# Kernel optimization log

Hardware: AMD Instinct MI355X
Metric: run time of the kernel (lower is better)

Reference implementation:

```python
import jax, jax.numpy as jnp
import numpy as np

B, D, H, L, T = 4096, 1024, 2048, 256, 8
STD = 0.02


def setup_inputs() -> dict:
    key = jax.random.key(0)
    ks = jax.random.split(key, 24)
    n = lambda k, shp: (jax.random.normal(k, shp, dtype=jnp.float32) * STD)
    inp = {
        "x": jax.random.uniform(ks[0], (B, D), dtype=jnp.float32),
        "task": jax.random.randint(ks[1], (B,), 0, T),
        "eps": jax.random.normal(ks[2], (B, L), dtype=jnp.float32),
        # per-task encoder stacks: in->H->H->H->2L
        "enc_W1": n(ks[3], (T, D, H)), "enc_b1": jnp.zeros((T, H)),
        "enc_W2": n(ks[4], (T, H, H)), "enc_b2": jnp.zeros((T, H)),
        "enc_W3": n(ks[5], (T, H, H)), "enc_b3": jnp.zeros((T, H)),
        "enc_W4": n(ks[6], (T, H, 2 * L)), "enc_b4": jnp.zeros((T, 2 * L)),
        # shared decoder (BayesianLinear means): L->H->H
        "ds_W1": n(ks[7], (L, H)), "ds_b1": jnp.zeros((H,)),
        "ds_W2": n(ks[8], (H, H)), "ds_b2": jnp.zeros((H,)),
        # per-task decoder heads: H->H->D with Sigmoid
        "hd_W1": n(ks[9], (T, H, H)), "hd_b1": jnp.zeros((T, H)),
        "hd_W2": n(ks[10], (T, H, D)), "hd_b2": jnp.zeros((T, D)),
    }
    return inp


def reference(x, task, eps,
              enc_W1, enc_b1, enc_W2, enc_b2, enc_W3, enc_b3, enc_W4, enc_b4,
              ds_W1, ds_b1, ds_W2, ds_b2,
              hd_W1, hd_b1, hd_W2, hd_b2):
    ntasks = enc_W1.shape[0]
    onehot = jax.nn.one_hot(task, ntasks, dtype=x.dtype)  # [B, T], the task==idx mask

    # ---- encode: run every task's encoder on the full batch, mask-sum ----
    def enc_one(W1, b1, W2, b2, W3, b3, W4, b4):
        h = jax.nn.relu(x @ W1 + b1)
        h = jax.nn.relu(h @ W2 + b2)
        h = jax.nn.relu(h @ W3 + b3)
        return h @ W4 + b4  # [B, 2L]

    enc_all = jax.vmap(enc_one)(enc_W1, enc_b1, enc_W2, enc_b2,
                                enc_W3, enc_b3, enc_W4, enc_b4)  # [T, B, 2L]
    scat = jnp.einsum('tbd,bt->bd', enc_all, onehot)  # [B, 2L]
    latent = scat.shape[1] // 2
    mu, log_sigma = scat[:, :latent], scat[:, latent:]
    z = mu + jnp.exp(log_sigma) * eps  # reparameterization

    # ---- decode: shared trunk, then every head masked ----
    h = jax.nn.relu(z @ ds_W1 + ds_b1)
    h = jax.nn.relu(h @ ds_W2 + ds_b2)  # [B, H]

    def head_one(W1, b1, W2, b2):
        g = jax.nn.relu(h @ W1 + b1)
        return jax.nn.sigmoid(g @ W2 + b2)  # [B, D]

    heads_all = jax.vmap(head_one)(hd_W1, hd_b1, hd_W2, hd_b2)  # [T, B, D]
    return jnp.einsum('tbd,bt->bd', heads_all, onehot)  # [B, D]
```

## Files before the change

### kernel.cpp

```cpp
#include <hip/hip_runtime.h>
#include <hip/hip_bf16.h>

#define T_TASKS 8
#define B_ROWS 4096
#define PADROWS 4224
#define BM 128
#define BN 128
#define BK 32
#define MAXTILES 40

typedef __attribute__((ext_vector_type(4))) float f32x4;
typedef __attribute__((ext_vector_type(8))) short bf16x8;

#define GLOAD_LDS16(g, l) __builtin_amdgcn_global_load_lds( \
    (const __attribute__((address_space(1))) void*)(g), \
    (__attribute__((address_space(3))) void*)(l), 16, 0, 0)

struct TP { const float* src; unsigned short* dst; int K; int N; int ntiles; };

__device__ __forceinline__ unsigned short f32_to_bf16(float f) {
    union { float f; unsigned int u; } v; v.f = f;
    unsigned int r = v.u + 0x7FFF + ((v.u >> 16) & 1);
    return (unsigned short)(r >> 16);
}

__global__ void setup_kernel(const int* __restrict__ task, int* __restrict__ perm,
                             int* __restrict__ offs, int* __restrict__ table) {
    __shared__ int cnt[T_TASKS];
    __shared__ int cur[T_TASKS];
    int tid = threadIdx.x;
    if (tid < T_TASKS) cnt[tid] = 0;
    __syncthreads();
    for (int b = tid; b < B_ROWS; b += blockDim.x)
        atomicAdd(&cnt[task[b]], 1);
    __syncthreads();
    if (tid == 0) {
        int o = 0;
        for (int t = 0; t < T_TASKS; ++t) { offs[t] = o; cur[t] = o; o += cnt[t]; }
        offs[T_TASKS] = o;
        int s = 0;
        for (int t = 0; t < T_TASKS; ++t) {
            int nt = (cnt[t] + BM - 1) / BM;
            for (int j = 0; j < nt; ++j) table[s++] = (t << 16) | j;
        }
        for (; s < MAXTILES; ++s) table[s] = -1;
    }
    __syncthreads();
    for (int b = tid; b < B_ROWS; b += blockDim.x) {
        int t = task[b];
        int pos = atomicAdd(&cur[t], 1);
        perm[pos] = b;
    }
}

__global__ void permute_cast_kernel(const float* __restrict__ x, const int* __restrict__ perm,
                                    unsigned short* __restrict__ xp) {
    int rowp = blockIdx.x;
    int src = perm[rowp];
    const float4* xin = reinterpret_cast<const float4*>(x + (size_t)src * 1024);
    unsigned short* dst = xp + (size_t)rowp * 1024;
    int c4 = threadIdx.x;
    float4 v = xin[c4];
    ushort4 o;
    o.x = f32_to_bf16(v.x); o.y = f32_to_bf16(v.y);
    o.z = f32_to_bf16(v.z); o.w = f32_to_bf16(v.w);
    *reinterpret_cast<ushort4*>(dst + c4 * 4) = o;
}

__global__ void vae_kernel(const float* __restrict__ scat, const float* __restrict__ eps,
                           const int* __restrict__ perm, unsigned short* __restrict__ z) {
    int rowp = blockIdx.x;
    int c = threadIdx.x;
    int src = perm[rowp];
    float mu = scat[(size_t)rowp * 512 + c];
    float ls = scat[(size_t)rowp * 512 + 256 + c];
    float e  = eps[(size_t)src * 256 + c];
    z[(size_t)rowp * 256 + c] = f32_to_bf16(mu + __expf(ls) * e);
}

__global__ __launch_bounds__(256)
void transpose_cast_kernel(const float* __restrict__ W, unsigned short* __restrict__ Wt,
                           int K, int N) {
    const size_t toff = (size_t)blockIdx.z * K * N;
    const float* Ws = W + toff;
    unsigned short* Wd = Wt + toff;
    const int k0 = blockIdx.x * 64;
    const int n0 = blockIdx.y * 64;
    __shared__ unsigned short Tt[64 * 64];
    const int tid = threadIdx.x;
    const int n = tid & 63;
    const int kq = tid >> 6;
    #pragma unroll
    for (int i = 0; i < 4; ++i) {
        int kk = kq * 16 + i * 4;
        const float* p = Ws + (size_t)(k0 + kk) * N + n0 + n;
        float v0 = p[0];
        float v1 = p[(size_t)N];
        float v2 = p[(size_t)2 * N];
        float v3 = p[(size_t)3 * N];
        unsigned int lo = (unsigned int)f32_to_bf16(v0) | ((unsigned int)f32_to_bf16(v1) << 16);
        unsigned int hi = (unsigned int)f32_to_bf16(v2) | ((unsigned int)f32_to_bf16(v3) << 16);
        int c = (kk >> 2) ^ (n & 15);
        *reinterpret_cast<uint2*>(Tt + n * 64 + c * 4) = make_uint2(lo, hi);
    }
    __syncthreads();
    #pragma unroll
    for (int it = 0; it < 2; ++it) {
        int c  = it * 256 + tid;
        int nn = c >> 3;
        int cg = c & 7;
        int c1 = (cg * 2) ^ (nn & 15);
        int c2 = (cg * 2 + 1) ^ (nn & 15);
        uint2 a = *reinterpret_cast<const uint2*>(Tt + nn * 64 + c1 * 4);
        uint2 b = *reinterpret_cast<const uint2*>(Tt + nn * 64 + c2 * 4);
        uint4 o = make_uint4(a.x, a.y, b.x, b.y);
        *reinterpret_cast<uint4*>(Wd + (size_t)(n0 + nn) * K + k0 + cg * 8) = o;
    }
}

template<int MODE>
__global__ __launch_bounds__(256, 2)
void gemm4_kernel(const unsigned short* __restrict__ A,
                  const unsigned short* __restrict__ Wt,
                  const float* __restrict__ bias, void* __restrict__ dst,
                  const int* __restrict__ offs, const int* __restrict__ table,
                  const int* __restrict__ perm,
                  int K, int N, int ldd, int Btot, int GX, TP tpa, TP tpb)
{
    __shared__ unsigned short lds[2][2][BM * BK];

    const int bx = blockIdx.x;
    const int tid = threadIdx.x;

    if (bx >= GX) {
        int tile = (bx - GX) * gridDim.y + blockIdx.y;
        const float* src; unsigned short* dstp; int tK, tN;
        if (tile < tpa.ntiles) { src = tpa.src; dstp = tpa.dst; tK = tpa.K; tN = tpa.N; }
        else {
            tile -= tpa.ntiles;
            if (tile >= tpb.ntiles) return;
            src = tpb.src; dstp = tpb.dst; tK = tpb.K; tN = tpb.N;
        }
        int tk = tK >> 6, tn = tN >> 6;
        int z = tile / (tk * tn);
        int r = tile % (tk * tn);
        int k0 = (r % tk) * 64, n0 = (r / tk) * 64;
        const size_t toff = (size_t)z * tK * tN;
        const float* Ws = src + toff;
        unsigned short* Wd = dstp + toff;
        unsigned short* Tt = &lds[0][0][0];
        const int n = tid & 63;
        const int kq = tid >> 6;
        #pragma unroll
        for (int i = 0; i < 4; ++i) {
            int kk = kq * 16 + i * 4;
            const float* p = Ws + (size_t)(k0 + kk) * tN + n0 + n;
            float v0 = p[0];
            float v1 = p[(size_t)tN];
            float v2 = p[(size_t)2 * tN];
            float v3 = p[(size_t)3 * tN];
            unsigned int lo = (unsigned int)f32_to_bf16(v0) | ((unsigned int)f32_to_bf16(v1) << 16);
            unsigned int hi = (unsigned int)f32_to_bf16(v2) | ((unsigned int)f32_to_bf16(v3) << 16);
            int c = (kk >> 2) ^ (n & 15);
            *reinterpret_cast<uint2*>(Tt + n * 64 + c * 4) = make_uint2(lo, hi);
        }
        __syncthreads();
        #pragma unroll
        for (int it = 0; it < 2; ++it) {
            int c  = it * 256 + tid;
            int nn = c >> 3;
            int cg = c & 7;
            int c1 = (cg * 2) ^ (nn & 15);
            int c2 = (cg * 2 + 1) ^ (nn & 15);
            uint2 a = *reinterpret_cast<const uint2*>(Tt + nn * 64 + c1 * 4);
            uint2 b = *reinterpret_cast<const uint2*>(Tt + nn * 64 + c2 * 4);
            uint4 o = make_uint4(a.x, a.y, b.x, b.y);
            *reinterpret_cast<uint4*>(Wd + (size_t)(n0 + nn) * tK + k0 + cg * 8) = o;
        }
        return;
    }

    int t, mtile, off, cnt;
    if (table != nullptr) {
        int v = table[bx];
        if (v < 0) return;
        t = v >> 16; mtile = v & 0xFFFF;
        off = offs[t]; cnt = offs[t + 1] - off;
    } else {
        t = 0; mtile = bx; off = 0; cnt = Btot;
    }
    const int n0 = blockIdx.y * BN;

    const int lane = tid & 63;
    const int wave = tid >> 6;
    const int wr = wave >> 1, wc = wave & 1;

    const int rl   = lane >> 2;
    const int csrc = ((lane & 3) ^ (rl & 3)) * 8;
    const unsigned short* Ab = A + ((size_t)(off + mtile * BM + rl)) * K + csrc;
    const unsigned short* Bb = Wt + ((size_t)t * N + n0 + rl) * K + csrc;

    auto stage = [&](int buf, int k0) {
        #pragma unroll
        for (int jj = 0; jj < 2; ++jj) {
            int j = wave * 2 + jj;
            GLOAD_LDS16(Ab + (size_t)(j * 16) * K + k0, &lds[buf][0][j * 512]);
            GLOAD_LDS16(Bb + (size_t)(j * 16) * K + k0, &lds[buf][1][j * 512]);
        }
    };

    f32x4 acc[4][4];
    #pragma unroll
    for (int m = 0; m < 4; ++m)
        #pragma unroll
        for (int n = 0; n < 4; ++n)
            acc[m][n] = (f32x4){0.f, 0.f, 0.f, 0.f};

    auto compute = [&](int buf) {
        bf16x8 af[4], bfr[4];
        #pragma unroll
        for (int m = 0; m < 4; ++m) {
            int rf = wr * 64 + m * 16 + (lane & 15);
            af[m] = *reinterpret_cast<const bf16x8*>(
                &lds[buf][0][rf * 32 + (((lane >> 4) ^ (rf & 3)) * 8)]);
        }
        #pragma unroll
        for (int n = 0; n < 4; ++n) {
            int nf = wc * 64 + n * 16 + (lane & 15);
            bfr[n] = *reinterpret_cast<const bf16x8*>(
                &lds[buf][1][nf * 32 + (((lane >> 4) ^ (nf & 3)) * 8)]);
        }
        #pragma unroll
        for (int m = 0; m < 4; ++m)
            #pragma unroll
            for (int n = 0; n < 4; ++n)
                acc[m][n] = __builtin_amdgcn_mfma_f32_16x16x32_bf16(af[m], bfr[n], acc[m][n], 0, 0, 0);
    };

    const int nsteps = K / BK;
    stage(0, 0);
    __syncthreads();
    int cur = 0;
    for (int s = 0; s < nsteps; ++s) {
        if (s + 1 < nsteps) stage(cur ^ 1, (s + 1) * BK);
        compute(cur);
        __syncthreads();
        cur ^= 1;
    }

    const float* bt = bias + (size_t)t * N;
    #pragma unroll
    for (int n = 0; n < 4; ++n) {
        int col = n0 + wc * 64 + n * 16 + (lane & 15);
        float bv = bt[col];
        #pragma unroll
        for (int m = 0; m < 4; ++m) {
            int rbase = mtile * BM + wr * 64 + m * 16 + ((lane >> 4) << 2);
            #pragma unroll
            for (int j = 0; j < 4; ++j) {
                int local = rbase + j;
                if (local >= cnt) continue;
                float v = acc[m][n][j] + bv;
                if (MODE == 0) {
                    ((unsigned short*)dst)[(size_t)(off + local) * ldd + col] =
                        f32_to_bf16(fmaxf(v, 0.f));
                } else if (MODE == 1) {
                    ((float*)dst)[(size_t)(off + local) * ldd + col] = v;
                } else {
                    int grow = perm[off + local];
                    ((float*)dst)[(size_t)grow * ldd + col] = 1.f / (1.f + __expf(-v));
                }
            }
        }
    }
}

extern "C" void kernel_launch(void* const* d_in, const int* in_sizes, int n_in,
                              void* d_out, int out_size, void* d_ws, size_t ws_size,
                              hipStream_t stream) {
    const float* x      = (const float*)d_in[0];
    const int*   task   = (const int*)d_in[1];
    const float* eps    = (const float*)d_in[2];
    const float* enc_W1 = (const float*)d_in[3];
    const float* enc_b1 = (const float*)d_in[4];
    const float* enc_W2 = (const float*)d_in[5];
    const float* enc_b2 = (const float*)d_in[6];
    const float* enc_W3 = (const float*)d_in[7];
    const float* enc_b3 = (const float*)d_in[8];
    const float* enc_W4 = (const float*)d_in[9];
    const float* enc_b4 = (const float*)d_in[10];
    const float* ds_W1  = (const float*)d_in[11];
    const float* ds_b1  = (const float*)d_in[12];
    const float* ds_W2  = (const float*)d_in[13];
    const float* ds_b2  = (const float*)d_in[14];
    const float* hd_W1  = (const float*)d_in[15];
    const float* hd_b1  = (const float*)d_in[16];
    const float* hd_W2  = (const float*)d_in[17];
    const float* hd_b2  = (const float*)d_in[18];
    float* out = (float*)d_out;

    char* ws = (char*)d_ws;
    int* perm  = (int*)ws;
    int* offs  = (int*)(ws + 16384);
    int* table = (int*)(ws + 16384 + 256);
    char* p = ws + 32768;
    unsigned short* xp = (unsigned short*)p; p += (size_t)PADROWS * 1024 * 2;
    unsigned short* h1 = (unsigned short*)p; p += (size_t)PADROWS * 2048 * 2;
    unsigned short* h2 = (unsigned short*)p; p += (size_t)PADROWS * 2048 * 2;
    unsigned short* zb = (unsigned short*)p; p += (size_t)PADROWS * 256 * 2;
    unsigned short* tw1  = (unsigned short*)p; p += (size_t)8 * 2048 * 1024 * 2;
    unsigned short* tw2  = (unsigned short*)p; p += (size_t)8 * 2048 * 2048 * 2;
    unsigned short* tw3  = (unsigned short*)p; p += (size_t)8 * 2048 * 2048 * 2;
    unsigned short* tw4  = (unsigned short*)p; p += (size_t)8 * 512 * 2048 * 2;
    unsigned short* tds1 = (unsigned short*)p; p += (size_t)2048 * 256 * 2;
    unsigned short* tds2 = (unsigned short*)p; p += (size_t)2048 * 2048 * 2;
    unsigned short* thd1 = (unsigned short*)p; p += (size_t)8 * 2048 * 2048 * 2;
    unsigned short* thd2 = (unsigned short*)p; p += (size_t)8 * 1024 * 2048 * 2;
    float* scat = out;

    const TP tnone = { nullptr, nullptr, 64, 64, 0 };
    const TP tpW2  = { enc_W2, tw2, 2048, 2048, 8192 };
    const TP tpW3  = { enc_W3, tw3, 2048, 2048, 8192 };
    const TP tpW4  = { enc_W4, tw4, 2048,  512, 2048 };
    const TP tpDS1 = { ds_W1, tds1,  256, 2048,  128 };
    const TP tpDS2 = { ds_W2, tds2, 2048, 2048, 1024 };
    const TP tpHD1 = { hd_W1, thd1, 2048, 2048, 8192 };
    const TP tpHD2 = { hd_W2, thd2, 2048, 1024, 4096 };

    setup_kernel<<<1, 1024, 0, stream>>>(task, perm, offs, table);
    permute_cast_kernel<<<B_ROWS, 256, 0, stream>>>(x, perm, xp);

    transpose_cast_kernel<<<dim3(16, 32, 8), 256, 0, stream>>>(enc_W1, tw1, 1024, 2048);

    gemm4_kernel<0><<<dim3(MAXTILES + 512, 16), 256, 0, stream>>>(xp, tw1, enc_b1, h1, offs, table, nullptr, 1024, 2048, 2048, B_ROWS, MAXTILES, tpW2, tnone);
    gemm4_kernel<0><<<dim3(MAXTILES + 512, 16), 256, 0, stream>>>(h1, tw2, enc_b2, h2, offs, table, nullptr, 2048, 2048, 2048, B_ROWS, MAXTILES, tpW3, tnone);
    gemm4_kernel<0><<<dim3(MAXTILES + 136, 16), 256, 0, stream>>>(h2, tw3, enc_b3, h1, offs, table, nullptr, 2048, 2048, 2048, B_ROWS, MAXTILES, tpW4, tpDS1);
    gemm4_kernel<1><<<dim3(MAXTILES + 256, 4), 256, 0, stream>>>(h1, tw4, enc_b4, scat, offs, table, nullptr, 2048, 512, 512, B_ROWS, MAXTILES, tpDS2, tnone);

    vae_kernel<<<B_ROWS, 256, 0, stream>>>(scat, eps, perm, zb);

    gemm4_kernel<0><<<dim3(32 + 512, 16), 256, 0, stream>>>(zb, tds1, ds_b1, h2, nullptr, nullptr, nullptr, 256, 2048, 2048, B_ROWS, 32, tpHD1, tnone);
    gemm4_kernel<0><<<dim3(32 + 256, 16), 256, 0, stream>>>(h2, tds2, ds_b2, h1, nullptr, nullptr, nullptr, 2048, 2048, 2048, B_ROWS, 32, tpHD2, tnone);

    gemm4_kernel<0><<<dim3(MAXTILES, 16), 256, 0, stream>>>(h1, thd1, hd_b1, h2, offs, table, nullptr, 2048, 2048, 2048, B_ROWS, MAXTILES, tnone, tnone);
    gemm4_kernel<2><<<dim3(MAXTILES, 8), 256, 0, stream>>>(h2, thd2, hd_b2, out, offs, table, perm, 2048, 1024, 1024, B_ROWS, MAXTILES, tnone, tnone);
}
```

Baseline: 663.7 us.

## Shrink GEMM N-tile to 64, raise occupancy, swizzle block order by row tile

Halves the GEMM output tile width from 128 to 64 columns and doubles the grid in y, which lets more blocks run per CU (launch bounds 4). It also remaps block x indices so neighbouring blocks work on different row tiles, and changes the LDS XOR swizzle to use (row>>1)&3. The transpose side-work is spread over the larger y grid with fewer x blocks. The aim is better occupancy and load balance on the grouped GEMMs. The cost is less operand reuse per block: A tiles are loaded twice as often relative to the MFMA work.

```diff
diff --git a/kernel.cpp b/kernel.cpp
--- a/kernel.cpp
+++ b/kernel.cpp
@@ -5,7 +5,7 @@
 #define B_ROWS 4096
 #define PADROWS 4224
 #define BM 128
-#define BN 128
+#define BN 64
 #define BK 32
 #define MAXTILES 40
 
@@ -119,21 +119,22 @@
 }
 
 template<int MODE>
-__global__ __launch_bounds__(256, 2)
-void gemm4_kernel(const unsigned short* __restrict__ A,
+__global__ __launch_bounds__(256, 4)
+void gemm6_kernel(const unsigned short* __restrict__ A,
                   const unsigned short* __restrict__ Wt,
                   const float* __restrict__ bias, void* __restrict__ dst,
                   const int* __restrict__ offs, const int* __restrict__ table,
                   const int* __restrict__ perm,
                   int K, int N, int ldd, int Btot, int GX, TP tpa, TP tpb)
 {
-    __shared__ unsigned short lds[2][2][BM * BK];
-
-    const int bx = blockIdx.x;
+    __shared__ unsigned short As[2][BM * BK];
+    __shared__ unsigned short Bs[2][BN * BK];
+
+    const int bxh = blockIdx.x;
     const int tid = threadIdx.x;
 
-    if (bx >= GX) {
-        int tile = (bx - GX) * gridDim.y + blockIdx.y;
+    if (bxh >= GX) {
+        int tile = (bxh - GX) * gridDim.y + blockIdx.y;
         const float* src; unsigned short* dstp; int tK, tN;
         if (tile < tpa.ntiles) { src = tpa.src; dstp = tpa.dst; tK = tpa.K; tN = tpa.N; }
         else {
@@ -148,7 +149,7 @@
         const size_t toff = (size_t)z * tK * tN;
         const float* Ws = src + toff;
         unsigned short* Wd = dstp + toff;
-        unsigned short* Tt = &lds[0][0][0];
+        unsigned short* Tt = &As[0][0];
         const int n = tid & 63;
         const int kq = tid >> 6;
         #pragma unroll
@@ -180,6 +181,9 @@
         return;
     }
 
+    int bx = bxh;
+    if ((GX & 7) == 0) bx = (bxh & 7) * (GX >> 3) + (bxh >> 3);
+
     int t, mtile, off, cnt;
     if (table != nullptr) {
         int v = table[bx];
@@ -196,7 +200,7 @@
     const int wr = wave >> 1, wc = wave & 1;
 
     const int rl   = lane >> 2;
-    const int csrc = ((lane & 3) ^ (rl & 3)) * 8;
+    const int csrc = ((lane & 3) ^ ((rl >> 1) & 3)) * 8;
     const unsigned short* Ab = A + ((size_t)(off + mtile * BM + rl)) * K + csrc;
     const unsigned short* Bb = Wt + ((size_t)t * N + n0 + rl) * K + csrc;
 
@@ -204,36 +208,36 @@
         #pragma unroll
         for (int jj = 0; jj < 2; ++jj) {
             int j = wave * 2 + jj;
-            GLOAD_LDS16(Ab + (size_t)(j * 16) * K + k0, &lds[buf][0][j * 512]);
-            GLOAD_LDS16(Bb + (size_t)(j * 16) * K + k0, &lds[buf][1][j * 512]);
-        }
+            GLOAD_LDS16(Ab + (size_t)(j * 16) * K + k0, &As[buf][j * 512]);
+        }
+        GLOAD_LDS16(Bb + (size_t)(wave * 16) * K + k0, &Bs[buf][wave * 512]);
     };
 
-    f32x4 acc[4][4];
+    f32x4 acc[4][2];
     #pragma unroll
     for (int m = 0; m < 4; ++m)
         #pragma unroll
-        for (int n = 0; n < 4; ++n)
+        for (int n = 0; n < 2; ++n)
             acc[m][n] = (f32x4){0.f, 0.f, 0.f, 0.f};
 
     auto compute = [&](int buf) {
-        bf16x8 af[4], bfr[4];
+        bf16x8 af[4], bfr[2];
         #pragma unroll
         for (int m = 0; m < 4; ++m) {
             int rf = wr * 64 + m * 16 + (lane & 15);
             af[m] = *reinterpret_cast<const bf16x8*>(
-                &lds[buf][0][rf * 32 + (((lane >> 4) ^ (rf & 3)) * 8)]);
-        }
-        #pragma unroll
-        for (int n = 0; n < 4; ++n) {
-            int nf = wc * 64 + n * 16 + (lane & 15);
+                &As[buf][rf * 32 + (((lane >> 4) ^ ((rf >> 1) & 3)) * 8)]);
+        }
+        #pragma unroll
+        for (int n = 0; n < 2; ++n) {
+            int nf = wc * 32 + n * 16 + (lane & 15);
             bfr[n] = *reinterpret_cast<const bf16x8*>(
-                &lds[buf][1][nf * 32 + (((lane >> 4) ^ (nf & 3)) * 8)]);
+                &Bs[buf][nf * 32 + (((lane >> 4) ^ ((nf >> 1) & 3)) * 8)]);
         }
         #pragma unroll
         for (int m = 0; m < 4; ++m)
             #pragma unroll
-            for (int n = 0; n < 4; ++n)
+            for (int n = 0; n < 2; ++n)
                 acc[m][n] = __builtin_amdgcn_mfma_f32_16x16x32_bf16(af[m], bfr[n], acc[m][n], 0, 0, 0);
     };
 
@@ -250,8 +254,8 @@
 
     const float* bt = bias + (size_t)t * N;
     #pragma unroll
-    for (int n = 0; n < 4; ++n) {
-        int col = n0 + wc * 64 + n * 16 + (lane & 15);
+    for (int n = 0; n < 2; ++n) {
+        int col = n0 + wc * 32 + n * 16 + (lane & 15);
         float bv = bt[col];
         #pragma unroll
         for (int m = 0; m < 4; ++m) {
@@ -332,16 +336,16 @@
 
     transpose_cast_kernel<<<dim3(16, 32, 8), 256, 0, stream>>>(enc_W1, tw1, 1024, 2048);
 
-    gemm4_kernel<0><<<dim3(MAXTILES + 512, 16), 256, 0, stream>>>(xp, tw1, enc_b1, h1, offs, table, nullptr, 1024, 2048, 2048, B_ROWS, MAXTILES, tpW2, tnone);
-    gemm4_kernel<0><<<dim3(MAXTILES + 512, 16), 256, 0, stream>>>(h1, tw2, enc_b2, h2, offs, table, nullptr, 2048, 2048, 2048, B_ROWS, MAXTILES, tpW3, tnone);
-    gemm4_kernel<0><<<dim3(MAXTILES + 136, 16), 256, 0, stream>>>(h2, tw3, enc_b3, h1, offs, table, nullptr, 2048, 2048, 2048, B_ROWS, MAXTILES, tpW4, tpDS1);
-    gemm4_kernel<1><<<dim3(MAXTILES + 256, 4), 256, 0, stream>>>(h1, tw4, enc_b4, scat, offs, table, nullptr, 2048, 512, 512, B_ROWS, MAXTILES, tpDS2, tnone);
+    gemm6_kernel<0><<<dim3(296, 32), 256, 0, stream>>>(xp, tw1, enc_b1, h1, offs, table, nullptr, 1024, 2048, 2048, B_ROWS, MAXTILES, tpW2, tnone);
+    gemm6_kernel<0><<<dim3(296, 32), 256, 0, stream>>>(h1, tw2, enc_b2, h2, offs, table, nullptr, 2048, 2048, 2048, B_ROWS, MAXTILES, tpW3, tnone);
+    gemm6_kernel<0><<<dim3(112, 32), 256, 0, stream>>>(h2, tw3, enc_b3, h1, offs, table, nullptr, 2048, 2048, 2048, B_ROWS, MAXTILES, tpW4, tpDS1);
+    gemm6_kernel<1><<<dim3(168, 8), 256, 0, stream>>>(h1, tw4, enc_b4, scat, offs, table, nullptr, 2048, 512, 512, B_ROWS, MAXTILES, tpDS2, tnone);
 
     vae_kernel<<<B_ROWS, 256, 0, stream>>>(scat, eps, perm, zb);
 
-    gemm4_kernel<0><<<dim3(32 + 512, 16), 256, 0, stream>>>(zb, tds1, ds_b1, h2, nullptr, nullptr, nullptr, 256, 2048, 2048, B_ROWS, 32, tpHD1, tnone);
-    gemm4_kernel<0><<<dim3(32 + 256, 16), 256, 0, stream>>>(h2, tds2, ds_b2, h1, nullptr, nullptr, nullptr, 2048, 2048, 2048, B_ROWS, 32, tpHD2, tnone);
-
-    gemm4_kernel<0><<<dim3(MAXTILES, 16), 256, 0, stream>>>(h1, thd1, hd_b1, h2, offs, table, nullptr, 2048, 2048, 2048, B_ROWS, MAXTILES, tnone, tnone);
-    gemm4_kernel<2><<<dim3(MAXTILES, 8), 256, 0, stream>>>(h2, thd2, hd_b2, out, offs, table, perm, 2048, 1024, 1024, B_ROWS, MAXTILES, tnone, tnone);
-}
+    gemm6_kernel<0><<<dim3(288, 32), 256, 0, stream>>>(zb, tds1, ds_b1, h2, nullptr, nullptr, nullptr, 256, 2048, 2048, B_ROWS, 32, tpHD1, tnone);
+    gemm6_kernel<0><<<dim3(160, 32), 256, 0, stream>>>(h2, tds2, ds_b2, h1, nullptr, nullptr, nullptr, 2048, 2048, 2048, B_ROWS, 32, tpHD2, tnone);
+
+    gemm6_kernel<0><<<dim3(MAXTILES, 32), 256, 0, stream>>>(h1, thd1, hd_b1, h2, offs, table, nullptr, 2048, 2048, 2048, B_ROWS, MAXTILES, tnone, tnone);
+    gemm6_kernel<2><<<dim3(MAXTILES, 16), 256, 0, stream>>>(h2, thd2, hd_b2, out, offs, table, perm, 2048, 1024, 1024, B_ROWS, MAXTILES, tnone, tnone);
+}
```

Result: slower. 692.0 us (+4.3%).

## Load MFMA fragments directly from global memory and remap tile order

Applied to the files above, without the earlier changes.

The GEMM kernel drops LDS staging via global_load_lds and instead has each wave load its bf16x8 MFMA fragments straight from global memory into registers, double-buffered in two register sets. This removes the per-step LDS round trip and __syncthreads. The cost is that waves no longer share A and B tiles, so global/L2 traffic per block grows and reads become 16-byte strided rows. It also remaps blockIdx.x to interleave M-tiles across groups of eight, which may change the tile-to-CU assignment.

```diff
diff --git a/kernel.cpp b/kernel.cpp
--- a/kernel.cpp
+++ b/kernel.cpp
@@ -11,10 +11,6 @@
 
 typedef __attribute__((ext_vector_type(4))) float f32x4;
 typedef __attribute__((ext_vector_type(8))) short bf16x8;
-
-#define GLOAD_LDS16(g, l) __builtin_amdgcn_global_load_lds( \
-    (const __attribute__((address_space(1))) void*)(g), \
-    (__attribute__((address_space(3))) void*)(l), 16, 0, 0)
 
 struct TP { const float* src; unsigned short* dst; int K; int N; int ntiles; };
 
@@ -120,20 +116,20 @@
 
 template<int MODE>
 __global__ __launch_bounds__(256, 2)
-void gemm4_kernel(const unsigned short* __restrict__ A,
-                  const unsigned short* __restrict__ Wt,
-                  const float* __restrict__ bias, void* __restrict__ dst,
-                  const int* __restrict__ offs, const int* __restrict__ table,
-                  const int* __restrict__ perm,
-                  int K, int N, int ldd, int Btot, int GX, TP tpa, TP tpb)
+void gemm13_kernel(const unsigned short* __restrict__ A,
+                   const unsigned short* __restrict__ Wt,
+                   const float* __restrict__ bias, void* __restrict__ dst,
+                   const int* __restrict__ offs, const int* __restrict__ table,
+                   const int* __restrict__ perm,
+                   int K, int N, int ldd, int Btot, int GX, TP tpa, TP tpb)
 {
-    __shared__ unsigned short lds[2][2][BM * BK];
-
-    const int bx = blockIdx.x;
+    __shared__ unsigned short Tt[64 * 64];
+
+    const int bxh = blockIdx.x;
     const int tid = threadIdx.x;
 
-    if (bx >= GX) {
-        int tile = (bx - GX) * gridDim.y + blockIdx.y;
+    if (bxh >= GX) {
+        int tile = (bxh - GX) * gridDim.y + blockIdx.y;
         const float* src; unsigned short* dstp; int tK, tN;
         if (tile < tpa.ntiles) { src = tpa.src; dstp = tpa.dst; tK = tpa.K; tN = tpa.N; }
         else {
@@ -148,7 +144,6 @@
         const size_t toff = (size_t)z * tK * tN;
         const float* Ws = src + toff;
         unsigned short* Wd = dstp + toff;
-        unsigned short* Tt = &lds[0][0][0];
         const int n = tid & 63;
         const int kq = tid >> 6;
         #pragma unroll
@@ -180,6 +175,8 @@
         return;
     }
 
+    int bx = (bxh & 7) * (GX >> 3) + (bxh >> 3);
+
     int t, mtile, off, cnt;
     if (table != nullptr) {
         int v = table[bx];
@@ -195,18 +192,18 @@
     const int wave = tid >> 6;
     const int wr = wave >> 1, wc = wave & 1;
 
-    const int rl   = lane >> 2;
-    const int csrc = ((lane & 3) ^ (rl & 3)) * 8;
-    const unsigned short* Ab = A + ((size_t)(off + mtile * BM + rl)) * K + csrc;
-    const unsigned short* Bb = Wt + ((size_t)t * N + n0 + rl) * K + csrc;
-
-    auto stage = [&](int buf, int k0) {
-        #pragma unroll
-        for (int jj = 0; jj < 2; ++jj) {
-            int j = wave * 2 + jj;
-            GLOAD_LDS16(Ab + (size_t)(j * 16) * K + k0, &lds[buf][0][j * 512]);
-            GLOAD_LDS16(Bb + (size_t)(j * 16) * K + k0, &lds[buf][1][j * 512]);
-        }
+    const unsigned short* Abase =
+        A + ((size_t)(off + mtile * BM + wr * 64 + (lane & 15))) * K + (lane >> 4) * 8;
+    const unsigned short* Bbase =
+        Wt + ((size_t)t * N + n0 + wc * 64 + (lane & 15)) * K + (lane >> 4) * 8;
+
+    auto lf = [&](bf16x8 (&a)[4], bf16x8 (&b)[4], int k0) {
+        #pragma unroll
+        for (int m = 0; m < 4; ++m)
+            a[m] = *reinterpret_cast<const bf16x8*>(Abase + (size_t)(m * 16) * K + k0);
+        #pragma unroll
+        for (int n = 0; n < 4; ++n)
+            b[n] = *reinterpret_cast<const bf16x8*>(Bbase + (size_t)(n * 16) * K + k0);
     };
 
     f32x4 acc[4][4];
@@ -216,36 +213,22 @@
         for (int n = 0; n < 4; ++n)
             acc[m][n] = (f32x4){0.f, 0.f, 0.f, 0.f};
 
-    auto compute = [&](int buf) {
-        bf16x8 af[4], bfr[4];
-        #pragma unroll
-        for (int m = 0; m < 4; ++m) {
-            int rf = wr * 64 + m * 16 + (lane & 15);
-            af[m] = *reinterpret_cast<const bf16x8*>(
-                &lds[buf][0][rf * 32 + (((lane >> 4) ^ (rf & 3)) * 8)]);
-        }
-        #pragma unroll
-        for (int n = 0; n < 4; ++n) {
-            int nf = wc * 64 + n * 16 + (lane & 15);
-            bfr[n] = *reinterpret_cast<const bf16x8*>(
-                &lds[buf][1][nf * 32 + (((lane >> 4) ^ (nf & 3)) * 8)]);
-        }
+    auto cm = [&](bf16x8 (&a)[4], bf16x8 (&b)[4]) {
         #pragma unroll
         for (int m = 0; m < 4; ++m)
             #pragma unroll
             for (int n = 0; n < 4; ++n)
-                acc[m][n] = __builtin_amdgcn_mfma_f32_16x16x32_bf16(af[m], bfr[n], acc[m][n], 0, 0, 0);
+                acc[m][n] = __builtin_amdgcn_mfma_f32_16x16x32_bf16(a[m], b[n], acc[m][n], 0, 0, 0);
     };
 
+    bf16x8 a0[4], b0[4], a1[4], b1[4];
     const int nsteps = K / BK;
-    stage(0, 0);
-    __syncthreads();
-    int cur = 0;
-    for (int s = 0; s < nsteps; ++s) {
-        if (s + 1 < nsteps) stage(cur ^ 1, (s + 1) * BK);
-        compute(cur);
-        __syncthreads();
-        cur ^= 1;
+    lf(a0, b0, 0);
+    for (int s = 0; s < nsteps; s += 2) {
+        if (s + 1 < nsteps) lf(a1, b1, (s + 1) * BK);
+        cm(a0, b0);
+        if (s + 2 < nsteps) lf(a0, b0, (s + 2) * BK);
+        cm(a1, b1);
     }
 
     const float* bt = bias + (size_t)t * N;
@@ -332,16 +315,16 @@
 
     transpose_cast_kernel<<<dim3(16, 32, 8), 256, 0, stream>>>(enc_W1, tw1, 1024, 2048);
 
-    gemm4_kernel<0><<<dim3(MAXTILES + 512, 16), 256, 0, stream>>>(xp, tw1, enc_b1, h1, offs, table, nullptr, 1024, 2048, 2048, B_ROWS, MAXTILES, tpW2, tnone);
-    gemm4_kernel<0><<<dim3(MAXTILES + 512, 16), 256, 0, stream>>>(h1, tw2, enc_b2, h2, offs, table, nullptr, 2048, 2048, 2048, B_ROWS, MAXTILES, tpW3, tnone);
-    gemm4_kernel<0><<<dim3(MAXTILES + 136, 16), 256, 0, stream>>>(h2, tw3, enc_b3, h1, offs, table, nullptr, 2048, 2048, 2048, B_ROWS, MAXTILES, tpW4, tpDS1);
-    gemm4_kernel<1><<<dim3(MAXTILES + 256, 4), 256, 0, stream>>>(h1, tw4, enc_b4, scat, offs, table, nullptr, 2048, 512, 512, B_ROWS, MAXTILES, tpDS2, tnone);
+    gemm13_kernel<0><<<dim3(552, 16), 256, 0, stream>>>(xp, tw1, enc_b1, h1, offs, table, nullptr, 1024, 2048, 2048, B_ROWS, MAXTILES, tpW2, tnone);
+    gemm13_kernel<0><<<dim3(552, 16), 256, 0, stream>>>(h1, tw2, enc_b2, h2, offs, table, nullptr, 2048, 2048, 2048, B_ROWS, MAXTILES, tpW3, tnone);
+    gemm13_kernel<0><<<dim3(176, 16), 256, 0, stream>>>(h2, tw3, enc_b3, h1, offs, table, nullptr, 2048, 2048, 2048, B_ROWS, MAXTILES, tpW4, tpDS1);
+    gemm13_kernel<1><<<dim3(296, 4), 256, 0, stream>>>(h1, tw4, enc_b4, scat, offs, table, nullptr, 2048, 512, 512, B_ROWS, MAXTILES, tpDS2, tnone);
 
     vae_kernel<<<B_ROWS, 256, 0, stream>>>(scat, eps, perm, zb);
 
-    gemm4_kernel<0><<<dim3(32 + 512, 16), 256, 0, stream>>>(zb, tds1, ds_b1, h2, nullptr, nullptr, nullptr, 256, 2048, 2048, B_ROWS, 32, tpHD1, tnone);
-    gemm4_kernel<0><<<dim3(32 + 256, 16), 256, 0, stream>>>(h2, tds2, ds_b2, h1, nullptr, nullptr, nullptr, 2048, 2048, 2048, B_ROWS, 32, tpHD2, tnone);
-
-    gemm4_kernel<0><<<dim3(MAXTILES, 16), 256, 0, stream>>>(h1, thd1, hd_b1, h2, offs, table, nullptr, 2048, 2048, 2048, B_ROWS, MAXTILES, tnone, tnone);
-    gemm4_kernel<2><<<dim3(MAXTILES, 8), 256, 0, stream>>>(h2, thd2, hd_b2, out, offs, table, perm, 2048, 1024, 1024, B_ROWS, MAXTILES, tnone, tnone);
-}
+    gemm13_kernel<0><<<dim3(544, 16), 256, 0, stream>>>(zb, tds1, ds_b1, h2, nullptr, nullptr, nullptr, 256, 2048, 2048, B_ROWS, 32, tpHD1, tnone);
+    gemm13_kernel<0><<<dim3(288, 16), 256, 0, stream>>>(h2, tds2, ds_b2, h1, nullptr, nullptr, nullptr, 2048, 2048, 2048, B_ROWS, 32, tpHD2, tnone);
+
+    gemm13_kernel<0><<<dim3(MAXTILES, 16), 256, 0, stream>>>(h1, thd1, hd_b1, h2, offs, table, nullptr, 2048, 2048, 2048, B_ROWS, MAXTILES, tnone, tnone);
+    gemm13_kernel<2><<<dim3(MAXTILES, 8), 256, 0, stream>>>(h2, thd2, hd_b2, out, offs, table, perm, 2048, 1024, 1024, B_ROWS, MAXTILES, tnone, tnone);
+}
```

After: 1.421 ms. +114.0%, slower.

## Triple-buffer GEMM LDS pipeline with vmcnt waits, new swizzle and tile remap

Applied to the files above, without the earlier changes.

Replaces the double-buffered loop with a three-stage LDS ring. Loads are issued two steps ahead, and s_waitcnt vmcnt plus a single barrier per step replace the two syncthreads. The LDS XOR swizzle is changed to use row>>1, and GEMM blocks are remapped across groups of 8 to change scheduling locality. The occupancy hint is raised to 3 blocks per CU, at the cost of more LDS per block and register pressure.

```diff
diff --git a/kernel.cpp b/kernel.cpp
--- a/kernel.cpp
+++ b/kernel.cpp
@@ -15,6 +15,9 @@
 #define GLOAD_LDS16(g, l) __builtin_amdgcn_global_load_lds( \
     (const __attribute__((address_space(1))) void*)(g), \
     (__attribute__((address_space(3))) void*)(l), 16, 0, 0)
+
+#define WAITV4() asm volatile("s_waitcnt vmcnt(4)" ::: "memory")
+#define WAITV0() asm volatile("s_waitcnt vmcnt(0)" ::: "memory")
 
 struct TP { const float* src; unsigned short* dst; int K; int N; int ntiles; };
 
@@ -119,21 +122,22 @@
 }
 
 template<int MODE>
-__global__ __launch_bounds__(256, 2)
-void gemm4_kernel(const unsigned short* __restrict__ A,
-                  const unsigned short* __restrict__ Wt,
-                  const float* __restrict__ bias, void* __restrict__ dst,
-                  const int* __restrict__ offs, const int* __restrict__ table,
-                  const int* __restrict__ perm,
-                  int K, int N, int ldd, int Btot, int GX, TP tpa, TP tpb)
+__global__ __launch_bounds__(256, 3)
+void gemm14_kernel(const unsigned short* __restrict__ A,
+                   const unsigned short* __restrict__ Wt,
+                   const float* __restrict__ bias, void* __restrict__ dst,
+                   const int* __restrict__ offs, const int* __restrict__ table,
+                   const int* __restrict__ perm,
+                   int K, int N, int ldd, int Btot, int GX, TP tpa, TP tpb)
 {
-    __shared__ unsigned short lds[2][2][BM * BK];
-
-    const int bx = blockIdx.x;
+    __shared__ unsigned short As[3][BM * BK];
+    __shared__ unsigned short Bs[3][BN * BK];
+
+    const int bxh = blockIdx.x;
     const int tid = threadIdx.x;
 
-    if (bx >= GX) {
-        int tile = (bx - GX) * gridDim.y + blockIdx.y;
+    if (bxh >= GX) {
+        int tile = (bxh - GX) * gridDim.y + blockIdx.y;
         const float* src; unsigned short* dstp; int tK, tN;
         if (tile < tpa.ntiles) { src = tpa.src; dstp = tpa.dst; tK = tpa.K; tN = tpa.N; }
         else {
@@ -148,7 +152,7 @@
         const size_t toff = (size_t)z * tK * tN;
         const float* Ws = src + toff;
         unsigned short* Wd = dstp + toff;
-        unsigned short* Tt = &lds[0][0][0];
+        unsigned short* Tt = &As[0][0];
         const int n = tid & 63;
         const int kq = tid >> 6;
         #pragma unroll
@@ -180,6 +184,8 @@
         return;
     }
 
+    int bx = (bxh & 7) * (GX >> 3) + (bxh >> 3);
+
     int t, mtile, off, cnt;
     if (table != nullptr) {
         int v = table[bx];
@@ -196,7 +202,7 @@
     const int wr = wave >> 1, wc = wave & 1;
 
     const int rl   = lane >> 2;
-    const int csrc = ((lane & 3) ^ (rl & 3)) * 8;
+    const int csrc = ((lane & 3) ^ ((rl >> 1) & 3)) * 8;
     const unsigned short* Ab = A + ((size_t)(off + mtile * BM + rl)) * K + csrc;
     const unsigned short* Bb = Wt + ((size_t)t * N + n0 + rl) * K + csrc;
 
@@ -204,8 +210,12 @@
         #pragma unroll
         for (int jj = 0; jj < 2; ++jj) {
             int j = wave * 2 + jj;
-            GLOAD_LDS16(Ab + (size_t)(j * 16) * K + k0, &lds[buf][0][j * 512]);
-            GLOAD_LDS16(Bb + (size_t)(j * 16) * K + k0, &lds[buf][1][j * 512]);
+            GLOAD_LDS16(Ab + (size_t)(j * 16) * K + k0, &As[buf][j * 512]);
+        }
+        #pragma unroll
+        for (int jb = 0; jb < 2; ++jb) {
+            int j = wave * 2 + jb;
+            GLOAD_LDS16(Bb + (size_t)(j * 16) * K + k0, &Bs[buf][j * 512]);
         }
     };
 
@@ -222,13 +232,13 @@
         for (int m = 0; m < 4; ++m) {
             int rf = wr * 64 + m * 16 + (lane & 15);
             af[m] = *reinterpret_cast<const bf16x8*>(
-                &lds[buf][0][rf * 32 + (((lane >> 4) ^ (rf & 3)) * 8)]);
+                &As[buf][rf * 32 + (((lane >> 4) ^ ((rf >> 1) & 3)) * 8)]);
         }
         #pragma unroll
         for (int n = 0; n < 4; ++n) {
             int nf = wc * 64 + n * 16 + (lane & 15);
             bfr[n] = *reinterpret_cast<const bf16x8*>(
-                &lds[buf][1][nf * 32 + (((lane >> 4) ^ (nf & 3)) * 8)]);
+                &Bs[buf][nf * 32 + (((lane >> 4) ^ ((nf >> 1) & 3)) * 8)]);
         }
         #pragma unroll
         for (int m = 0; m < 4; ++m)
@@ -239,14 +249,21 @@
 
     const int nsteps = K / BK;
     stage(0, 0);
-    __syncthreads();
+    stage(1, BK);
     int cur = 0;
-    for (int s = 0; s < nsteps; ++s) {
-        if (s + 1 < nsteps) stage(cur ^ 1, (s + 1) * BK);
+    for (int s = 0; s < nsteps - 1; ++s) {
+        WAITV4();
+        __builtin_amdgcn_s_barrier();
+        if (s + 2 < nsteps) {
+            int tgt = cur + 2; if (tgt >= 3) tgt -= 3;
+            stage(tgt, (s + 2) * BK);
+        }
         compute(cur);
-        __syncthreads();
-        cur ^= 1;
-    }
+        ++cur; if (cur == 3) cur = 0;
+    }
+    WAITV0();
+    __builtin_amdgcn_s_barrier();
+    compute(cur);
 
     const float* bt = bias + (size_t)t * N;
     #pragma unroll
@@ -332,16 +349,16 @@
 
     transpose_cast_kernel<<<dim3(16, 32, 8), 256, 0, stream>>>(enc_W1, tw1, 1024, 2048);
 
-    gemm4_kernel<0><<<dim3(MAXTILES + 512, 16), 256, 0, stream>>>(xp, tw1, enc_b1, h1, offs, table, nullptr, 1024, 2048, 2048, B_ROWS, MAXTILES, tpW2, tnone);
-    gemm4_kernel<0><<<dim3(MAXTILES + 512, 16), 256, 0, stream>>>(h1, tw2, enc_b2, h2, offs, table, nullptr, 2048, 2048, 2048, B_ROWS, MAXTILES, tpW3, tnone);
-    gemm4_kernel<0><<<dim3(MAXTILES + 136, 16), 256, 0, stream>>>(h2, tw3, enc_b3, h1, offs, table, nullptr, 2048, 2048, 2048, B_ROWS, MAXTILES, tpW4, tpDS1);
-    gemm4_kernel<1><<<dim3(MAXTILES + 256, 4), 256, 0, stream>>>(h1, tw4, enc_b4, scat, offs, table, nullptr, 2048, 512, 512, B_ROWS, MAXTILES, tpDS2, tnone);
+    gemm14_kernel<0><<<dim3(552, 16), 256, 0, stream>>>(xp, tw1, enc_b1, h1, offs, table, nullptr, 1024, 2048, 2048, B_ROWS, MAXTILES, tpW2, tnone);
+    gemm14_kernel<0><<<dim3(552, 16), 256, 0, stream>>>(h1, tw2, enc_b2, h2, offs, table, nullptr, 2048, 2048, 2048, B_ROWS, MAXTILES, tpW3, tnone);
+    gemm14_kernel<0><<<dim3(176, 16), 256, 0, stream>>>(h2, tw3, enc_b3, h1, offs, table, nullptr, 2048, 2048, 2048, B_ROWS, MAXTILES, tpW4, tpDS1);
+    gemm14_kernel<1><<<dim3(296, 4), 256, 0, stream>>>(h1, tw4, enc_b4, scat, offs, table, nullptr, 2048, 512, 512, B_ROWS, MAXTILES, tpDS2, tnone);
 
     vae_kernel<<<B_ROWS, 256, 0, stream>>>(scat, eps, perm, zb);
 
-    gemm4_kernel<0><<<dim3(32 + 512, 16), 256, 0, stream>>>(zb, tds1, ds_b1, h2, nullptr, nullptr, nullptr, 256, 2048, 2048, B_ROWS, 32, tpHD1, tnone);
-    gemm4_kernel<0><<<dim3(32 + 256, 16), 256, 0, stream>>>(h2, tds2, ds_b2, h1, nullptr, nullptr, nullptr, 2048, 2048, 2048, B_ROWS, 32, tpHD2, tnone);
-
-    gemm4_kernel<0><<<dim3(MAXTILES, 16), 256, 0, stream>>>(h1, thd1, hd_b1, h2, offs, table, nullptr, 2048, 2048, 2048, B_ROWS, MAXTILES, tnone, tnone);
-    gemm4_kernel<2><<<dim3(MAXTILES, 8), 256, 0, stream>>>(h2, thd2, hd_b2, out, offs, table, perm, 2048, 1024, 1024, B_ROWS, MAXTILES, tnone, tnone);
-}
+    gemm14_kernel<0><<<dim3(544, 16), 256, 0, stream>>>(zb, tds1, ds_b1, h2, nullptr, nullptr, nullptr, 256, 2048, 2048, B_ROWS, 32, tpHD1, tnone);
+    gemm14_kernel<0><<<dim3(288, 16), 256, 0, stream>>>(h2, tds2, ds_b2, h1, nullptr, nullptr, nullptr, 2048, 2048, 2048, B_ROWS, 32, tpHD2, tnone);
+
+    gemm14_kernel<0><<<dim3(MAXTILES, 16), 256, 0, stream>>>(h1, thd1, hd_b1, h2, offs, table, nullptr, 2048, 2048, 2048, B_ROWS, MAXTILES, tnone, tnone);
+    gemm14_kernel<2><<<dim3(MAXTILES, 8), 256, 0, stream>>>(h2, thd2, hd_b2, out, offs, table, perm, 2048, 1024, 1024, B_ROWS, MAXTILES, tnone, tnone);
+}
```

New measurement: 652.7 us. About the same (-1.7%).
